# Kernel optimization log

Hardware: AMD Instinct MI355X
Metric: run time of the kernel (lower is better)

The kernel has to match this reference:

```python
import jax, jax.numpy as jnp
import numpy as np
from jax import lax

V_PATCH = (1, 2, 3, 4, 5, 6, 8, 10, 13, 16)
BETA = 0.25
RESI = 0.5          # abs(quant_resi): h*(1-r) + conv(h)*r
K_PHI = 4           # share_quant_resi
PHI_TICKS = np.linspace(1.0 / (3 * K_PHI), 1.0 - 1.0 / (3 * K_PHI), K_PHI)


def _area_mat(out_s, in_s):
    # torch F.interpolate(mode='area') == adaptive avg pool: row-stochastic matrix
    M = np.zeros((out_s, in_s), np.float32)
    for i in range(out_s):
        s = (i * in_s) // out_s
        e = -((-(i + 1) * in_s) // out_s)  # ceil((i+1)*in/out)
        M[i, s:e] = 1.0 / (e - s)
    return jnp.asarray(M)


def _bicubic_mat(out_s, in_s):
    # torch bicubic, align_corners=False, a=-0.75, border-clamped taps
    a = -0.75
    i = np.arange(out_s)
    src = (i + 0.5) * in_s / out_s - 0.5
    fl = np.floor(src)
    M = np.zeros((out_s, in_s), np.float32)
    for t in range(-1, 3):
        x = np.abs(src - (fl + t))
        w = np.where(x <= 1.0, (a + 2) * x**3 - (a + 3) * x**2 + 1.0,
                     np.where(x < 2.0, a * x**3 - 5 * a * x**2 + 8 * a * x - 4 * a, 0.0))
        idx = np.clip(fl + t, 0, in_s - 1).astype(int)
        np.add.at(M, (i, idx), w)
    return jnp.asarray(M)


def _resize(x, M):
    # separable resize on square maps: x [B,C,h,w] -> [B,C,o,o]
    x = jnp.einsum('oh,bchw->bcow', M, x)
    return jnp.einsum('pw,bcow->bcop', M, x)


def _phi(h, w, b):
    # Phi: Conv2d(C,C,3,pad=1); out = h*(1-r) + conv(h)*r
    c = lax.conv_general_dilated(h, w, (1, 1), 'SAME',
                                 dimension_numbers=('NCHW', 'OIHW', 'NCHW'))
    c = c + b[None, :, None, None]
    return h * (1.0 - RESI) + c * RESI


def setup_inputs() -> dict:
    key = jax.random.key(0)
    k1, k2, k3, k4 = jax.random.split(key, 4)
    f = jax.random.normal(k1, (128, 32, 16, 16), jnp.float32)
    emb = jax.random.normal(k2, (4096, 32), jnp.float32) * 0.1
    phi_w = jax.random.normal(k3, (4, 32, 32, 3, 3), jnp.float32) * 0.05
    phi_b = jax.random.normal(k4, (4, 32), jnp.float32) * 0.01
    return {"f_BChw": f, "emb_W": emb, "phi_W": phi_w, "phi_b": phi_b}


def reference(f_BChw, emb_W, phi_W, phi_b):
    B, C, H, W = f_BChw.shape
    SN = len(V_PATCH)
    f = f_BChw.astype(jnp.float32)
    f_ng = lax.stop_gradient(f)
    f_rest = f_ng
    f_hat = jnp.zeros_like(f_ng)
    emb_ng = lax.stop_gradient(emb_W)         # torch uses embedding.weight.data
    e_sq = jnp.sum(emb_ng**2, axis=1)          # [V]
    loss = jnp.float32(0.0)
    idx_list = []
    for si, pn in enumerate(V_PATCH):
        rest = f_rest if si == SN - 1 else _resize(f_rest, _area_mat(pn, H))
        rest_NC = rest.transpose(0, 2, 3, 1).reshape(-1, C)      # [B*pn*pn, C]
        d = jnp.sum(rest_NC**2, axis=1, keepdims=True) + e_sq - 2.0 * (rest_NC @ emb_ng.T)
        idx = jnp.argmin(d, axis=1)                              # [B*pn*pn]
        idx_list.append(idx)
        h = emb_W[idx].reshape(B, pn, pn, C).transpose(0, 3, 1, 2)  # differentiable gather
        if si != SN - 1:
            h = _resize(h, _bicubic_mat(H, pn))
        k = int(np.argmin(np.abs(PHI_TICKS - si / (SN - 1))))
        h = _phi(h, phi_W[k], phi_b[k])
        f_hat = f_hat + h
        f_rest = f_rest - h
        loss = loss + BETA * jnp.mean((lax.stop_gradient(f_hat) - f)**2) \
                    + jnp.mean((f_hat - f_ng)**2)
    loss = loss / SN
    f_hat_out = lax.stop_gradient(f_hat) - f_ng + f  # straight-through
    return (f_hat_out, loss, jnp.concatenate(idx_list))
```

## Files before the change

kernel.cpp:

```cpp
#include <hip/hip_runtime.h>
#include <hip/hip_bf16.h>
#include <math.h>


#define B_  128
#define V_  4096
#define SN_ 10
#define NPIX_ (B_*32*256)

#define WS_FREST   0
#define WS_SLOTA   1048576
#define WS_SLOTB   1114112
#define WS_ESQ     1179648
#define WS_TW      1183744
#define WS_TI      1184320
#define WS_LOSSP   1184896
#define WS_RESTH   1187456
#define WS_RESTM   1711744
#define WS_RESTL   2236032
#define WS_EMBH    2760320
#define WS_EMBM    2825856
#define WS_EMBL    2891392
#define WS_WSPL    2956928

typedef __attribute__((ext_vector_type(8))) short short8_t;
typedef __attribute__((ext_vector_type(4))) float f32x4;
typedef unsigned long long ull;
#define MFMA(a,b,c) __builtin_amdgcn_mfma_f32_16x16x32_bf16((a),(b),(c),0,0,0)

__device__ inline void gl_lds16(const void* g, void* l) {
  __builtin_amdgcn_global_load_lds((const __attribute__((address_space(1))) void*)g,
                                   (__attribute__((address_space(3))) void*)l, 16, 0, 0);
}
__device__ inline void gl_lds4(const void* g, void* l) {
  __builtin_amdgcn_global_load_lds((const __attribute__((address_space(1))) void*)g,
                                   (__attribute__((address_space(3))) void*)l, 4, 0, 0);
}

__device__ inline void split3(float a, ushort* h, ushort* m, ushort* l) {
  unsigned ua = __float_as_uint(a);
  ushort uh = (ushort)(ua >> 16);
  float fh = __uint_as_float((unsigned)uh << 16);
  float r1 = a - fh;
  ushort um = (ushort)(__float_as_uint(r1) >> 16);
  float fm = __uint_as_float((unsigned)um << 16);
  float r2 = r1 - fm;
  ushort ul = (ushort)(__float_as_uint(r2) >> 16);
  *h = uh; *m = um; *l = ul;
}

__device__ inline short8_t s8_from_laneM1(short8_t v) {
  union { short8_t s; unsigned u[4]; } a, r;
  a.s = v;
#pragma unroll
  for (int i = 0; i < 4; ++i)
    r.u[i] = __builtin_amdgcn_update_dpp(0u, a.u[i], 0x111, 0xF, 0xF, true);
  return r.s;
}
__device__ inline short8_t s8_from_laneP1(short8_t v) {
  union { short8_t s; unsigned u[4]; } a, r;
  a.s = v;
#pragma unroll
  for (int i = 0; i < 4; ++i)
    r.u[i] = __builtin_amdgcn_update_dpp(0u, a.u[i], 0x101, 0xF, 0xF, true);
  return r.s;
}


__global__ __launch_bounds__(256) void k_prep(const float* __restrict__ emb,
                                              float* __restrict__ esq,
                                              ushort* __restrict__ eh,
                                              ushort* __restrict__ em,
                                              ushort* __restrict__ el,
                                              float* __restrict__ tw,
                                              int* __restrict__ ti,
                                              ull* __restrict__ slotA) {
  int bx = blockIdx.x, t = threadIdx.x;
  if (bx < 16) {
    int v = bx * 256 + t;
    const float4* e4 = (const float4*)(emb + (size_t)v * 32);
    float s = 0.f;
#pragma unroll
    for (int half = 0; half < 4; ++half) {
      float4 x0 = e4[half * 2], x1 = e4[half * 2 + 1];
      s += x0.x * x0.x + x0.y * x0.y + x0.z * x0.z + x0.w * x0.w;
      s += x1.x * x1.x + x1.y * x1.y + x1.z * x1.z + x1.w * x1.w;
      float xs[8] = {x0.x, x0.y, x0.z, x0.w, x1.x, x1.y, x1.z, x1.w};
      ushort hs[8], ms[8], ls[8];
#pragma unroll
      for (int j = 0; j < 8; ++j) split3(xs[j], &hs[j], &ms[j], &ls[j]);
      uint4 ph, pm, pl;
      ph.x = (unsigned)hs[0] | ((unsigned)hs[1] << 16); ph.y = (unsigned)hs[2] | ((unsigned)hs[3] << 16);
      ph.z = (unsigned)hs[4] | ((unsigned)hs[5] << 16); ph.w = (unsigned)hs[6] | ((unsigned)hs[7] << 16);
      pm.x = (unsigned)ms[0] | ((unsigned)ms[1] << 16); pm.y = (unsigned)ms[2] | ((unsigned)ms[3] << 16);
      pm.z = (unsigned)ms[4] | ((unsigned)ms[5] << 16); pm.w = (unsigned)ms[6] | ((unsigned)ms[7] << 16);
      pl.x = (unsigned)ls[0] | ((unsigned)ls[1] << 16); pl.y = (unsigned)ls[2] | ((unsigned)ls[3] << 16);
      pl.z = (unsigned)ls[4] | ((unsigned)ls[5] << 16); pl.w = (unsigned)ls[6] | ((unsigned)ls[7] << 16);
      ((uint4*)(eh + (size_t)v * 32))[half] = ph;
      ((uint4*)(em + (size_t)v * 32))[half] = pm;
      ((uint4*)(el + (size_t)v * 32))[half] = pl;
    }
    esq[v] = -0.5f * s;
  } else {
    if (t < 128) slotA[t] = 0ULL;
    if (t >= 144) return;
    const int pns[9] = {1, 2, 3, 4, 5, 6, 8, 10, 13};
    int si = t / 16, Y = t % 16;
    int pn = pns[si];
    double src = (Y + 0.5) * (double)pn / 16.0 - 0.5;
    double fl = floor(src);
    const double a = -0.75;
#pragma unroll
    for (int k = 0; k < 4; ++k) {
      double x = fabs(src - (fl + (k - 1)));
      double w;
      if (x <= 1.0)      w = (a + 2.0) * x * x * x - (a + 3.0) * x * x + 1.0;
      else if (x < 2.0)  w = a * x * x * x - 5.0 * a * x * x + 8.0 * a * x - 4.0 * a;
      else               w = 0.0;
      int id = (int)fl + (k - 1);
      id = id < 0 ? 0 : (id > pn - 1 ? pn - 1 : id);
      tw[si * 64 + Y * 4 + k] = (float)w;
      ti[si * 64 + Y * 4 + k] = id;
    }
  }
}

__global__ __launch_bounds__(256) void k_prep2(const float* __restrict__ f,
                                               const float* __restrict__ phiW,
                                               ushort* __restrict__ rh,
                                               ushort* __restrict__ rm,
                                               ushort* __restrict__ rl,
                                               ushort* __restrict__ wspl) {
  int bx = blockIdx.x, t = threadIdx.x;
  if (bx < 16) {
    int i = bx * 256 + t;
    int phi = i >> 10, o = (i >> 5) & 31, ci = i & 31;
    const float* src = phiW + (((size_t)phi * 32 + o) * 32 + ci) * 9;
    ushort* dst = wspl + (size_t)phi * 27648;
#pragma unroll
    for (int q = 0; q < 9; ++q) {
      ushort uh, um, ul;
      split3(src[q], &uh, &um, &ul);
      dst[(size_t)(0 * 9 + q) * 1024 + o * 32 + ci] = uh;
      dst[(size_t)(9 + q) * 1024 + o * 32 + ci] = um;
      dst[(size_t)(18 + q) * 1024 + o * 32 + ci] = ul;
    }
  } else {
    int tid = (bx - 16) * 256 + t;
    int c = tid & 31, n = tid >> 5;
    const float* base = f + ((size_t)n * 32 + c) * 256;
    float s = 0.f;
    for (int yy = 0; yy < 16; ++yy)
      for (int xx = 0; xx < 16; ++xx) s += base[yy * 16 + xx];
    float a = s * ((1.0f / 16.0f) * (1.0f / 16.0f));
    ushort uh, um, ul;
    split3(a, &uh, &um, &ul);
    rh[(size_t)n * 32 + c] = uh;
    rm[(size_t)n * 32 + c] = um;
    rl[(size_t)n * 32 + c] = ul;
  }
}

template<int R>
__global__ __launch_bounds__(256) void k_nn(const ushort* __restrict__ rest_h,
                                            const ushort* __restrict__ rest_m,
                                            const ushort* __restrict__ rest_l,
                                            const ushort* __restrict__ emb_h,
                                            const ushort* __restrict__ emb_m,
                                            const ushort* __restrict__ emb_l,
                                            const float* __restrict__ esq_g,
                                            ull* __restrict__ slot,
                                            int rows, int S, int cps) {
  __shared__ ushort lb[2][3][2048];
  __shared__ float les[2][64];
  const int t = threadIdx.x;
  const int w = t >> 6;
  const int col = t & 15;
  const int g = (t >> 4) & 3;
  const int sp = blockIdx.y;
  const int rowbase = blockIdx.x * (64 * R);

  auto stage = [&](int bf, int ch) {
    int cb = sp * cps + ch * 64;
    int code = cb + (t >> 2);
    int u = (t & 3) ^ ((code ^ (code >> 2)) & 3);
    size_t off = (size_t)code * 32 + (size_t)u * 8;
    gl_lds16(emb_h + off, &lb[bf][0][w * 512]);
    gl_lds16(emb_m + off, &lb[bf][1][w * 512]);
    gl_lds16(emb_l + off, &lb[bf][2][w * 512]);
    if ((t & 63) < 16) gl_lds4(esq_g + cb + w * 16 + (t & 15), &les[bf][w * 16]);
  };

  stage(0, 0);

  short8_t ah[R], am[R], al[R];
#pragma unroll
  for (int rt = 0; rt < R; ++rt) {
    int n = rowbase + (w * R + rt) * 16 + col;
    if (n >= rows) n = rows - 1;
    size_t o = (size_t)n * 32 + g * 8;
    ah[rt] = *(const short8_t*)(rest_h + o);
    am[rt] = *(const short8_t*)(rest_m + o);
    al[rt] = *(const short8_t*)(rest_l + o);
  }

  float best[R][4];
  int bidx[R][4];
#pragma unroll
  for (int rt = 0; rt < R; ++rt)
#pragma unroll
    for (int r = 0; r < 4; ++r) { best[rt][r] = -3.4e38f; bidx[rt][r] = 0x7fffffff; }

  const int NC = cps >> 6;
  int buf = 0;
  for (int ch = 0; ch < NC; ++ch) {
    if (ch + 1 < NC) {
      stage(buf ^ 1, ch + 1);
      asm volatile("s_waitcnt vmcnt(4)" ::: "memory");
    } else {
      asm volatile("s_waitcnt vmcnt(0)" ::: "memory");
    }
    __builtin_amdgcn_s_barrier();

    int cb0 = sp * cps + ch * 64;
#pragma unroll
    for (int s4 = 0; s4 < 4; ++s4) {
      int cl = s4 * 16 + col;
      int slotbase = (cl * 4 + (g ^ ((cl ^ (cl >> 2)) & 3))) * 8;
      short8_t bh  = *(const short8_t*)&lb[buf][0][slotbase];
      short8_t bm  = *(const short8_t*)&lb[buf][1][slotbase];
      short8_t bl2 = *(const short8_t*)&lb[buf][2][slotbase];
      float es = les[buf][cl];
      f32x4 c0 = {es, es, es, es};
      f32x4 acc[R];
#pragma unroll
      for (int rt = 0; rt < R; ++rt) acc[rt] = MFMA(ah[rt], bh, c0);
#pragma unroll
      for (int rt = 0; rt < R; ++rt) acc[rt] = MFMA(ah[rt], bm, acc[rt]);
#pragma unroll
      for (int rt = 0; rt < R; ++rt) acc[rt] = MFMA(am[rt], bh, acc[rt]);
#pragma unroll
      for (int rt = 0; rt < R; ++rt) acc[rt] = MFMA(ah[rt], bl2, acc[rt]);
#pragma unroll
      for (int rt = 0; rt < R; ++rt) acc[rt] = MFMA(am[rt], bm, acc[rt]);
#pragma unroll
      for (int rt = 0; rt < R; ++rt) acc[rt] = MFMA(al[rt], bh, acc[rt]);
      int code = cb0 + cl;
#pragma unroll
      for (int rt = 0; rt < R; ++rt)
#pragma unroll
        for (int r = 0; r < 4; ++r)
          if (acc[rt][r] > best[rt][r]) { best[rt][r] = acc[rt][r]; bidx[rt][r] = code; }
    }
    __syncthreads();
    buf ^= 1;
  }

#pragma unroll
  for (int rt = 0; rt < R; ++rt)
#pragma unroll
    for (int r = 0; r < 4; ++r) {
      float bd = best[rt][r];
      int bi = bidx[rt][r];
#pragma unroll
      for (int mm2 = 1; mm2 < 16; mm2 <<= 1) {
        float od = __shfl_xor(bd, mm2, 16);
        int oi = __shfl_xor(bi, mm2, 16);
        if (od > bd || (od == bd && oi < bi)) { bd = od; bi = oi; }
      }
      if ((t & 15) == 0) {
        int rown = rowbase + (w * R + rt) * 16 + g * 4 + r;
        if (rown < rows) {
          unsigned mu = __float_as_uint(bd);
          mu ^= (mu & 0x80000000u) ? 0xFFFFFFFFu : 0x80000000u;
          ull key = ((ull)mu << 32) | (unsigned)(~bi);
          atomicMax(&slot[rown], key);
        }
      }
    }
}

template<bool LAST>
__global__ __launch_bounds__(1024) void k_scale(const ull* __restrict__ slot_in,
                                                ull* __restrict__ slot_next,
                                                const float* __restrict__ emb,
                                                const float* __restrict__ tw,
                                                const int* __restrict__ ti,
                                                const ushort* __restrict__ wspl,
                                                const float* __restrict__ bias,
                                                const float* __restrict__ f,
                                                const float* __restrict__ fr_in,
                                                float* __restrict__ fr_out,
                                                float* __restrict__ fhat_out,
                                                float* __restrict__ out_idx_f,
                                                float* __restrict__ lossp,
                                                ushort* __restrict__ rh,
                                                ushort* __restrict__ rm,
                                                ushort* __restrict__ rl,
                                                int pn, int si, int pn_next,
                                                int rows_next) {
  __shared__ ushort h_bf[3][256][40];
  __shared__ float hsm[32 * 177];
  __shared__ float xt[32][208];
  __shared__ float h_my[16][260];
  __shared__ ushort w_lds[27][16][36];
  __shared__ int ci_s[256];
  __shared__ float redw[16];
  float* poolb = hsm;

  const int b = blockIdx.x;
  const int cog = blockIdx.y * 16;
  const int t = threadIdx.x;
  const int pn2 = pn * pn;
  const int w = t >> 6, l = t & 63;
  const int X = l & 15, kq = l >> 4;
  const int pix = w * 16 + X;

  float fr_old[4], f_old[4];
#pragma unroll
  for (int r = 0; r < 4; ++r) {
    size_t ga = ((size_t)b * 32 + cog + kq * 4 + r) * 256 + pix;
    fr_old[r] = fr_in[ga];
    f_old[r] = LAST ? f[ga] : 0.f;
  }
  for (int i = t; i < 1728; i += 1024) {
    int seg = i & 3;
    int o = (i >> 2) & 15;
    int lq = i >> 6;
    const ushort* src = wspl + ((size_t)lq * 32 + cog + o) * 32 + seg * 8;
    *(short8_t*)&w_lds[lq][o][seg * 8] = *(const short8_t*)src;
  }
  for (int rem = t; rem < pn2; rem += 1024) {
    ull sv = slot_in[b * pn2 + rem];
    int code = (int)(~(unsigned)sv);
    ci_s[rem] = code;
    out_idx_f[b * pn2 + rem] = (float)code;
  }
  __syncthreads();

  if (LAST) {
    const float4* emb4 = (const float4*)emb;
    for (int i = t; i < 2048; i += 1024) {
      int p2 = i >> 3, cq = i & 7;
      float4 e = emb4[(size_t)ci_s[p2] * 8 + cq];
      float vs[4] = {e.x, e.y, e.z, e.w};
#pragma unroll
      for (int j = 0; j < 4; ++j) {
        int c = cq * 4 + j;
        ushort uh, um, ul; split3(vs[j], &uh, &um, &ul);
        h_bf[0][p2][c] = uh; h_bf[1][p2][c] = um; h_bf[2][p2][c] = ul;
        int cl = c - cog;
        if ((unsigned)cl < 16u) h_my[cl][p2] = vs[j];
      }
    }
    __syncthreads();
  } else {
    const float4* emb4 = (const float4*)emb;
    for (int i = t; i < pn2 * 8; i += 1024) {
      int rem = i >> 3, cq = i & 7;
      float4 e = emb4[(size_t)ci_s[rem] * 8 + cq];
      hsm[(cq * 4 + 0) * 177 + rem] = e.x;
      hsm[(cq * 4 + 1) * 177 + rem] = e.y;
      hsm[(cq * 4 + 2) * 177 + rem] = e.z;
      hsm[(cq * 4 + 3) * 177 + rem] = e.w;
    }
    __syncthreads();

#pragma unroll
    for (int cc = 0; cc < 2; ++cc) {
      int c = 2 * w + cc;
      for (int i = l; i < pn * 16; i += 64) {
        int Xi = i & 15, y = i >> 4;
        float a = 0.f;
#pragma unroll
        for (int u = 0; u < 4; ++u)
          a += tw[si * 64 + Xi * 4 + u] * hsm[c * 177 + y * pn + ti[si * 64 + Xi * 4 + u]];
        xt[c][y * 16 + Xi] = a;
      }
      asm volatile("s_waitcnt lgkmcnt(0)" ::: "memory");
      for (int p2 = l; p2 < 256; p2 += 64) {
        int Xi = p2 & 15, Y = p2 >> 4;
        float a = 0.f;
#pragma unroll
        for (int u = 0; u < 4; ++u)
          a += tw[si * 64 + Y * 4 + u] * xt[c][ti[si * 64 + Y * 4 + u] * 16 + Xi];
        ushort uh, um, ul; split3(a, &uh, &um, &ul);
        h_bf[0][p2][c] = uh; h_bf[1][p2][c] = um; h_bf[2][p2][c] = ul;
        int cl = c - cog;
        if ((unsigned)cl < 16u) h_my[cl][p2] = a;
      }
    }
    __syncthreads();
  }

  f32x4 accA, accB;
#pragma unroll
  for (int r = 0; r < 4; ++r) {
    accA[r] = bias[cog + kq * 4 + r];
    accB[r] = 0.f;
  }

  for (int dy = 0; dy < 3; ++dy) {
    int Yp = w + dy - 1;
    bool ok = (Yp >= 0 && Yp < 16);
    short8_t bc[3];
    if (ok) {
#pragma unroll
      for (int lv = 0; lv < 3; ++lv)
        bc[lv] = *(const short8_t*)&h_bf[lv][Yp * 16 + X][kq * 8];
    }
#pragma unroll
    for (int dx = 0; dx < 3; ++dx) {
      int q = dy * 3 + dx;
      short8_t aH = *(const short8_t*)&w_lds[0 * 9 + q][l & 15][kq * 8];
      short8_t aM = *(const short8_t*)&w_lds[9 + q][l & 15][kq * 8];
      short8_t aL = *(const short8_t*)&w_lds[18 + q][l & 15][kq * 8];
      if (!ok) continue;
      short8_t bH = bc[0], bM = bc[1], bL = bc[2];
      if (dx == 0) { bH = s8_from_laneM1(bH); bM = s8_from_laneM1(bM); bL = s8_from_laneM1(bL); }
      else if (dx == 2) { bH = s8_from_laneP1(bH); bM = s8_from_laneP1(bM); bL = s8_from_laneP1(bL); }
      accA = MFMA(aH, bH, accA);
      accB = MFMA(aH, bM, accB);
      accA = MFMA(aM, bH, accA);
      accB = MFMA(aH, bL, accB);
      accA = MFMA(aM, bM, accA);
      accB = MFMA(aL, bH, accB);
    }
  }

  float lsum = 0.f;
#pragma unroll
  for (int r = 0; r < 4; ++r) {
    int ol = kq * 4 + r;
    float convv = accA[r] + accB[r];
    float outv = 0.5f * h_my[ol][pix] + 0.5f * convv;
    float nf = fr_old[r] - outv;
    size_t ga = ((size_t)b * 32 + cog + ol) * 256 + pix;
    if (LAST) {
      fhat_out[ga] = f_old[r] - nf;
    } else {
      fr_out[ga] = nf;
      poolb[ol * 256 + pix] = nf;
    }
    lsum += nf * nf;
  }

  if (!LAST) {
    __syncthreads();
    int pn2n = pn_next * pn_next;
    for (int i = t; i < 16 * pn2n; i += 1024) {
      int o = i & 15, rem = i >> 4;
      int y = rem / pn_next, x = rem - y * pn_next;
      int sy = (y * 16) / pn_next, ey = ((y + 1) * 16 + pn_next - 1) / pn_next;
      int sx = (x * 16) / pn_next, ex = ((x + 1) * 16 + pn_next - 1) / pn_next;
      float s = 0.f;
      for (int yy = sy; yy < ey; ++yy)
        for (int xx = sx; xx < ex; ++xx) s += poolb[o * 256 + yy * 16 + xx];
      float a = s * ((1.0f / (float)(ey - sy)) * (1.0f / (float)(ex - sx)));
      ushort uh, um, ul;
      split3(a, &uh, &um, &ul);
      size_t n = (size_t)b * pn2n + rem;
      rh[n * 32 + cog + o] = uh;
      rm[n * 32 + cog + o] = um;
      rl[n * 32 + cog + o] = ul;
    }
    int blk = b * 2 + blockIdx.y;
    int stride = (rows_next + 255) >> 8;
    int base = blk * stride;
    for (int i = t; i < stride; i += 1024) {
      int s = base + i;
      if (s < rows_next) slot_next[s] = 0ULL;
    }
  }

#pragma unroll
  for (int off = 32; off > 0; off >>= 1) lsum += __shfl_down(lsum, off);
  if (l == 0) redw[w] = lsum;
  __syncthreads();
  if (t == 0) {
    float s2 = 0.f;
#pragma unroll
    for (int i = 0; i < 16; ++i) s2 += redw[i];
    lossp[si * 256 + blockIdx.y * 128 + b] = s2;
  }
}

__global__ __launch_bounds__(256) void k_lossfin(const float* __restrict__ part,
                                                 float* __restrict__ out) {
  int t = threadIdx.x;
  float s = 0.f;
  for (int i = t; i < SN_ * 256; i += 256) s += part[i];
  __shared__ float red[256];
  red[t] = s;
  __syncthreads();
  for (int o = 128; o > 0; o >>= 1) {
    if (t < o) red[t] += red[t + o];
    __syncthreads();
  }
  if (t == 0) out[NPIX_] = red[0] * (1.25f / (10.0f * (float)NPIX_));
}


static void compute_phi_k(int* ks) {
  const int K = 4;
  double start = 1.0 / (3.0 * K);
  double stop = 1.0 - 1.0 / (3.0 * K);
  double step = (stop - start) / (K - 1);
  double ticks[4];
  for (int i = 0; i < K; ++i) ticks[i] = (double)i * step + start;
  ticks[K - 1] = stop;
  for (int si = 0; si < SN_; ++si) {
    double x = (double)si / (SN_ - 1);
    int best = 0;
    double bd = fabs(ticks[0] - x);
    for (int i = 1; i < K; ++i) {
      double d = fabs(ticks[i] - x);
      if (d < bd) { bd = d; best = i; }
    }
    ks[si] = best;
  }
}

extern "C" void kernel_launch(void* const* d_in, const int* in_sizes, int n_in,
                              void* d_out, int out_size, void* d_ws, size_t ws_size,
                              hipStream_t stream) {
  (void)in_sizes; (void)n_in; (void)out_size; (void)ws_size;
  const float* f    = (const float*)d_in[0];
  const float* emb  = (const float*)d_in[1];
  const float* phiW = (const float*)d_in[2];
  const float* phiB = (const float*)d_in[3];
  float* out = (float*)d_out;
  float* ws = (float*)d_ws;

  float* f_rest = ws + WS_FREST;
  ull*   slotA  = (ull*)(ws + WS_SLOTA);
  ull*   slotB  = (ull*)(ws + WS_SLOTB);
  float* esq    = ws + WS_ESQ;
  float* tw     = ws + WS_TW;
  int*   ti     = (int*)(ws + WS_TI);
  float* lossp  = ws + WS_LOSSP;
  ushort* rest_h = (ushort*)(ws + WS_RESTH);
  ushort* rest_m = (ushort*)(ws + WS_RESTM);
  ushort* rest_l = (ushort*)(ws + WS_RESTL);
  ushort* emb_h  = (ushort*)(ws + WS_EMBH);
  ushort* emb_m  = (ushort*)(ws + WS_EMBM);
  ushort* emb_l  = (ushort*)(ws + WS_EMBL);
  ushort* wspl   = (ushort*)(ws + WS_WSPL);

  static const int pns[SN_] = {1, 2, 3, 4, 5, 6, 8, 10, 13, 16};
  static const int Rs[SN_]  = {1, 1, 1, 2, 2, 2, 4, 4, 4, 4};
  static const int Ss[SN_]  = {64, 64, 32, 32, 16, 16, 16, 16, 8, 4};
  int ks[SN_];
  compute_phi_k(ks);

  k_prep<<<17, 256, 0, stream>>>(emb, esq, emb_h, emb_m, emb_l, tw, ti, slotA);
  k_prep2<<<32, 256, 0, stream>>>(f, phiW, rest_h, rest_m, rest_l, wspl);

  int idx_off = 0;
  for (int si = 0; si < SN_; ++si) {
    int pn = pns[si];
    int pn2 = pn * pn;
    int rows = B_ * pn2;
    int R = Rs[si], S = Ss[si];
    int cps = V_ / S;
    int rowblocks = (rows + 64 * R - 1) / (64 * R);
    ull* slot_cur  = (si & 1) ? slotB : slotA;
    ull* slot_nxt  = (si & 1) ? slotA : slotB;

    dim3 grid(rowblocks, S);
    if (R == 1)
      k_nn<1><<<grid, 256, 0, stream>>>(rest_h, rest_m, rest_l, emb_h, emb_m, emb_l,
                                        esq, slot_cur, rows, S, cps);
    else if (R == 2)
      k_nn<2><<<grid, 256, 0, stream>>>(rest_h, rest_m, rest_l, emb_h, emb_m, emb_l,
                                        esq, slot_cur, rows, S, cps);
    else
      k_nn<4><<<grid, 256, 0, stream>>>(rest_h, rest_m, rest_l, emb_h, emb_m, emb_l,
                                        esq, slot_cur, rows, S, cps);

    bool last = (si == SN_ - 1);
    int pn_next = last ? 0 : pns[si + 1];
    int rows_next = last ? 0 : B_ * pn_next * pn_next;
    const ushort* wsp = wspl + (size_t)ks[si] * 27648;
    const float* bi = phiB + (size_t)ks[si] * 32;
    if (last)
      k_scale<true><<<dim3(B_, 2), 1024, 0, stream>>>(
          slot_cur, slot_nxt, emb, tw, ti, wsp, bi, f,
          f_rest, f_rest, out,
          out + NPIX_ + 1 + idx_off, lossp,
          rest_h, rest_m, rest_l, pn, si, pn_next, rows_next);
    else
      k_scale<false><<<dim3(B_, 2), 1024, 0, stream>>>(
          slot_cur, slot_nxt, emb, tw, ti, wsp, bi, f,
          (si == 0) ? f : f_rest, f_rest, nullptr,
          out + NPIX_ + 1 + idx_off, lossp,
          rest_h, rest_m, rest_l, pn, si, pn_next, rows_next);
    idx_off += rows;
  }

  k_lossfin<<<1, 256, 0, stream>>>(lossp, out);
}
```

Before: 363.5 us.

## Split k_scale by image half, use fp32 rest with atomic area-pool accumulation

```diff
diff --git a/kernel.cpp b/kernel.cpp
--- a/kernel.cpp
+++ b/kernel.cpp
@@ -9,19 +9,18 @@
 #define NPIX_ (B_*32*256)
 
 #define WS_FREST   0
-#define WS_SLOTA   1048576
-#define WS_SLOTB   1114112
-#define WS_ESQ     1179648
-#define WS_TW      1183744
-#define WS_TI      1184320
-#define WS_LOSSP   1184896
-#define WS_RESTH   1187456
-#define WS_RESTM   1711744
-#define WS_RESTL   2236032
-#define WS_EMBH    2760320
-#define WS_EMBM    2825856
-#define WS_EMBL    2891392
-#define WS_WSPL    2956928
+#define WS_RF0     1048576
+#define WS_RF1     2097152
+#define WS_SLOTA   3145728
+#define WS_SLOTB   3211264
+#define WS_ESQ     3276800
+#define WS_TW      3280896
+#define WS_TI      3281472
+#define WS_LOSSP   3282048
+#define WS_EMBH    3287168
+#define WS_EMBM    3352704
+#define WS_EMBL    3418240
+#define WS_WSPL    3483776
 
 typedef __attribute__((ext_vector_type(8))) short short8_t;
 typedef __attribute__((ext_vector_type(4))) float f32x4;
@@ -74,7 +73,8 @@
                                               ushort* __restrict__ el,
                                               float* __restrict__ tw,
                                               int* __restrict__ ti,
-                                              ull* __restrict__ slotA) {
+                                              ull* __restrict__ slotA,
+                                              float* __restrict__ rf1) {
   int bx = blockIdx.x, t = threadIdx.x;
   if (bx < 16) {
     int v = bx * 256 + t;
@@ -103,6 +103,7 @@
     esq[v] = -0.5f * s;
   } else {
     if (t < 128) slotA[t] = 0ULL;
+    for (int i = t; i < 16384; i += 256) rf1[i] = 0.f;
     if (t >= 144) return;
     const int pns[9] = {1, 2, 3, 4, 5, 6, 8, 10, 13};
     int si = t / 16, Y = t % 16;
@@ -127,9 +128,7 @@
 
 __global__ __launch_bounds__(256) void k_prep2(const float* __restrict__ f,
                                                const float* __restrict__ phiW,
-                                               ushort* __restrict__ rh,
-                                               ushort* __restrict__ rm,
-                                               ushort* __restrict__ rl,
+                                               float* __restrict__ rf0,
                                                ushort* __restrict__ wspl) {
   int bx = blockIdx.x, t = threadIdx.x;
   if (bx < 16) {
@@ -152,19 +151,12 @@
     float s = 0.f;
     for (int yy = 0; yy < 16; ++yy)
       for (int xx = 0; xx < 16; ++xx) s += base[yy * 16 + xx];
-    float a = s * ((1.0f / 16.0f) * (1.0f / 16.0f));
-    ushort uh, um, ul;
-    split3(a, &uh, &um, &ul);
-    rh[(size_t)n * 32 + c] = uh;
-    rm[(size_t)n * 32 + c] = um;
-    rl[(size_t)n * 32 + c] = ul;
+    rf0[(size_t)n * 32 + c] = s * ((1.0f / 16.0f) * (1.0f / 16.0f));
   }
 }
 
 template<int R>
-__global__ __launch_bounds__(256) void k_nn(const ushort* __restrict__ rest_h,
-                                            const ushort* __restrict__ rest_m,
-                                            const ushort* __restrict__ rest_l,
+__global__ __launch_bounds__(256) void k_nn(const float* __restrict__ rest_f,
                                             const ushort* __restrict__ emb_h,
                                             const ushort* __restrict__ emb_m,
                                             const ushort* __restrict__ emb_l,
@@ -198,10 +190,14 @@
   for (int rt = 0; rt < R; ++rt) {
     int n = rowbase + (w * R + rt) * 16 + col;
     if (n >= rows) n = rows - 1;
-    size_t o = (size_t)n * 32 + g * 8;
-    ah[rt] = *(const short8_t*)(rest_h + o);
-    am[rt] = *(const short8_t*)(rest_m + o);
-    al[rt] = *(const short8_t*)(rest_l + o);
+    const float* rf = rest_f + (size_t)n * 32 + g * 8;
+    f32x4 v0 = *(const f32x4*)rf;
+    f32x4 v1 = *(const f32x4*)(rf + 4);
+    float vs[8] = {v0[0], v0[1], v0[2], v0[3], v1[0], v1[1], v1[2], v1[3]};
+    union { ushort u[8]; short8_t s; } H, M, L;
+#pragma unroll
+    for (int j = 0; j < 8; ++j) split3(vs[j], &H.u[j], &M.u[j], &L.u[j]);
+    ah[rt] = H.s; am[rt] = M.s; al[rt] = L.s;
   }
 
   float best[R][4];
@@ -281,41 +277,48 @@
 }
 
 template<bool LAST>
-__global__ __launch_bounds__(1024) void k_scale(const ull* __restrict__ slot_in,
-                                                ull* __restrict__ slot_next,
-                                                const float* __restrict__ emb,
-                                                const float* __restrict__ tw,
-                                                const int* __restrict__ ti,
-                                                const ushort* __restrict__ wspl,
-                                                const float* __restrict__ bias,
-                                                const float* __restrict__ f,
-                                                const float* __restrict__ fr_in,
-                                                float* __restrict__ fr_out,
-                                                float* __restrict__ fhat_out,
-                                                float* __restrict__ out_idx_f,
-                                                float* __restrict__ lossp,
-                                                ushort* __restrict__ rh,
-                                                ushort* __restrict__ rm,
-                                                ushort* __restrict__ rl,
-                                                int pn, int si, int pn_next,
-                                                int rows_next) {
-  __shared__ ushort h_bf[3][256][40];
-  __shared__ float hsm[32 * 177];
-  __shared__ float xt[32][208];
-  __shared__ float h_my[16][260];
+__global__ __launch_bounds__(512, 4) void k_scale(const ull* __restrict__ slot_in,
+                                                  ull* __restrict__ slot_next,
+                                                  float* __restrict__ rest_next,
+                                                  float* __restrict__ rest_zero,
+                                                  const float* __restrict__ emb,
+                                                  const float* __restrict__ tw,
+                                                  const int* __restrict__ ti,
+                                                  const ushort* __restrict__ wspl_k,
+                                                  const float* __restrict__ bias,
+                                                  const float* __restrict__ f,
+                                                  const float* __restrict__ fr_in,
+                                                  float* __restrict__ fr_out,
+                                                  float* __restrict__ fhat_out,
+                                                  float* __restrict__ out_idx_f,
+                                                  float* __restrict__ lossp,
+                                                  int pn, int si, int pn_next,
+                                                  int rows_next, int rows_z2) {
+  __shared__ ushort h_bf[3][144][32];
+  __shared__ float xt8[8][208];
+  __shared__ float hsm8[8][176];
+  __shared__ float h_my[16][128];
   __shared__ ushort w_lds[27][16][36];
   __shared__ int ci_s[256];
-  __shared__ float redw[16];
-  float* poolb = hsm;
+  __shared__ float redw[8];
 
   const int b = blockIdx.x;
   const int cog = blockIdx.y * 16;
+  const int z = blockIdx.z;
   const int t = threadIdx.x;
   const int pn2 = pn * pn;
   const int w = t >> 6, l = t & 63;
   const int X = l & 15, kq = l >> 4;
-  const int pix = w * 16 + X;
-
+  const int grow = z * 8 + w;
+  const int pix = grow * 16 + X;
+  const int rowbase = z ? 7 : 0;
+
+  for (int rem = t; rem < pn2; rem += 512) {
+    ull sv = slot_in[b * pn2 + rem];
+    int code = (int)(~(unsigned)sv);
+    ci_s[rem] = code;
+    if (blockIdx.y == 0 && z == 0) out_idx_f[b * pn2 + rem] = (float)code;
+  }
   float fr_old[4], f_old[4];
 #pragma unroll
   for (int r = 0; r < 4; ++r) {
@@ -323,74 +326,77 @@
     fr_old[r] = fr_in[ga];
     f_old[r] = LAST ? f[ga] : 0.f;
   }
-  for (int i = t; i < 1728; i += 1024) {
+  for (int i = t; i < 1728; i += 512) {
     int seg = i & 3;
     int o = (i >> 2) & 15;
     int lq = i >> 6;
-    const ushort* src = wspl + ((size_t)lq * 32 + cog + o) * 32 + seg * 8;
+    const ushort* src = wspl_k + ((size_t)lq * 32 + cog + o) * 32 + seg * 8;
     *(short8_t*)&w_lds[lq][o][seg * 8] = *(const short8_t*)src;
-  }
-  for (int rem = t; rem < pn2; rem += 1024) {
-    ull sv = slot_in[b * pn2 + rem];
-    int code = (int)(~(unsigned)sv);
-    ci_s[rem] = code;
-    out_idx_f[b * pn2 + rem] = (float)code;
   }
   __syncthreads();
 
   if (LAST) {
     const float4* emb4 = (const float4*)emb;
-    for (int i = t; i < 2048; i += 1024) {
-      int p2 = i >> 3, cq = i & 7;
-      float4 e = emb4[(size_t)ci_s[p2] * 8 + cq];
+    for (int i = t; i < 1152; i += 512) {
+      int lp = i % 144, cq = i / 144;
+      int gp = rowbase * 16 + lp;
+      float4 e = emb4[(size_t)ci_s[gp] * 8 + cq];
       float vs[4] = {e.x, e.y, e.z, e.w};
 #pragma unroll
       for (int j = 0; j < 4; ++j) {
         int c = cq * 4 + j;
         ushort uh, um, ul; split3(vs[j], &uh, &um, &ul);
-        h_bf[0][p2][c] = uh; h_bf[1][p2][c] = um; h_bf[2][p2][c] = ul;
+        int sc = (c & 7) + (((c >> 3) ^ (lp & 3)) << 3);
+        h_bf[0][lp][sc] = uh; h_bf[1][lp][sc] = um; h_bf[2][lp][sc] = ul;
+        int grr = rowbase + (lp >> 4);
         int cl = c - cog;
-        if ((unsigned)cl < 16u) h_my[cl][p2] = vs[j];
+        if ((unsigned)cl < 16u && (grr >> 3) == z)
+          h_my[cl][(grr - z * 8) * 16 + (lp & 15)] = vs[j];
       }
     }
     __syncthreads();
   } else {
     const float4* emb4 = (const float4*)emb;
-    for (int i = t; i < pn2 * 8; i += 1024) {
-      int rem = i >> 3, cq = i & 7;
-      float4 e = emb4[(size_t)ci_s[rem] * 8 + cq];
-      hsm[(cq * 4 + 0) * 177 + rem] = e.x;
-      hsm[(cq * 4 + 1) * 177 + rem] = e.y;
-      hsm[(cq * 4 + 2) * 177 + rem] = e.z;
-      hsm[(cq * 4 + 3) * 177 + rem] = e.w;
-    }
-    __syncthreads();
-
-#pragma unroll
-    for (int cc = 0; cc < 2; ++cc) {
-      int c = 2 * w + cc;
-      for (int i = l; i < pn * 16; i += 64) {
-        int Xi = i & 15, y = i >> 4;
+#pragma unroll 1
+    for (int P = 0; P < 4; ++P) {
+      for (int i = t; i < pn2 * 2; i += 512) {
+        int rem = i >> 1, hf = i & 1;
+        float4 e = emb4[(size_t)ci_s[rem] * 8 + P * 2 + hf];
+        hsm8[hf * 4 + 0][rem] = e.x;
+        hsm8[hf * 4 + 1][rem] = e.y;
+        hsm8[hf * 4 + 2][rem] = e.z;
+        hsm8[hf * 4 + 3][rem] = e.w;
+      }
+      __syncthreads();
+      int e1n = 8 * pn * 16;
+      for (int i = t; i < e1n; i += 512) {
+        int Xi = i & 15, r2 = i >> 4;
+        int y = r2 % pn, c8 = r2 / pn;
         float a = 0.f;
 #pragma unroll
         for (int u = 0; u < 4; ++u)
-          a += tw[si * 64 + Xi * 4 + u] * hsm[c * 177 + y * pn + ti[si * 64 + Xi * 4 + u]];
-        xt[c][y * 16 + Xi] = a;
-      }
-      asm volatile("s_waitcnt lgkmcnt(0)" ::: "memory");
-      for (int p2 = l; p2 < 256; p2 += 64) {
-        int Xi = p2 & 15, Y = p2 >> 4;
+          a += tw[si * 64 + Xi * 4 + u] * hsm8[c8][y * pn + ti[si * 64 + Xi * 4 + u]];
+        xt8[c8][y * 16 + Xi] = a;
+      }
+      __syncthreads();
+      for (int i = t; i < 1152; i += 512) {
+        int lp = i % 144, c8 = i / 144;
+        int Xi = lp & 15, lr = lp >> 4;
+        int gY = rowbase + lr;
         float a = 0.f;
 #pragma unroll
         for (int u = 0; u < 4; ++u)
-          a += tw[si * 64 + Y * 4 + u] * xt[c][ti[si * 64 + Y * 4 + u] * 16 + Xi];
+          a += tw[si * 64 + gY * 4 + u] * xt8[c8][ti[si * 64 + gY * 4 + u] * 16 + Xi];
+        int c = P * 8 + c8;
         ushort uh, um, ul; split3(a, &uh, &um, &ul);
-        h_bf[0][p2][c] = uh; h_bf[1][p2][c] = um; h_bf[2][p2][c] = ul;
+        int sc = (c & 7) + (((c >> 3) ^ (lp & 3)) << 3);
+        h_bf[0][lp][sc] = uh; h_bf[1][lp][sc] = um; h_bf[2][lp][sc] = ul;
         int cl = c - cog;
-        if ((unsigned)cl < 16u) h_my[cl][p2] = a;
-      }
-    }
-    __syncthreads();
+        if ((unsigned)cl < 16u && (gY >> 3) == z)
+          h_my[cl][(gY - z * 8) * 16 + Xi] = a;
+      }
+      __syncthreads();
+    }
   }
 
   f32x4 accA, accB;
@@ -401,13 +407,15 @@
   }
 
   for (int dy = 0; dy < 3; ++dy) {
-    int Yp = w + dy - 1;
-    bool ok = (Yp >= 0 && Yp < 16);
+    int gYp = grow + dy - 1;
+    bool ok = (gYp >= 0 && gYp < 16);
     short8_t bc[3];
     if (ok) {
+      int lp = (gYp - rowbase) * 16 + X;
+      int sc = ((kq ^ (lp & 3)) << 3);
 #pragma unroll
       for (int lv = 0; lv < 3; ++lv)
-        bc[lv] = *(const short8_t*)&h_bf[lv][Yp * 16 + X][kq * 8];
+        bc[lv] = *(const short8_t*)&h_bf[lv][lp][sc];
     }
 #pragma unroll
     for (int dx = 0; dx < 3; ++dx) {
@@ -428,48 +436,64 @@
     }
   }
 
+  float nf_r[4];
   float lsum = 0.f;
 #pragma unroll
   for (int r = 0; r < 4; ++r) {
     int ol = kq * 4 + r;
     float convv = accA[r] + accB[r];
-    float outv = 0.5f * h_my[ol][pix] + 0.5f * convv;
+    float outv = 0.5f * h_my[ol][w * 16 + X] + 0.5f * convv;
     float nf = fr_old[r] - outv;
     size_t ga = ((size_t)b * 32 + cog + ol) * 256 + pix;
     if (LAST) {
       fhat_out[ga] = f_old[r] - nf;
     } else {
       fr_out[ga] = nf;
-      poolb[ol * 256 + pix] = nf;
-    }
+    }
+    nf_r[r] = nf;
     lsum += nf * nf;
   }
 
   if (!LAST) {
     __syncthreads();
+    float* poolb = &h_my[0][0];
+#pragma unroll
+    for (int r = 0; r < 4; ++r)
+      poolb[(kq * 4 + r) * 128 + w * 16 + X] = nf_r[r];
+    __syncthreads();
     int pn2n = pn_next * pn_next;
-    for (int i = t; i < 16 * pn2n; i += 1024) {
+    int z8 = z * 8;
+    for (int i = t; i < 16 * pn2n; i += 512) {
       int o = i & 15, rem = i >> 4;
       int y = rem / pn_next, x = rem - y * pn_next;
       int sy = (y * 16) / pn_next, ey = ((y + 1) * 16 + pn_next - 1) / pn_next;
       int sx = (x * 16) / pn_next, ex = ((x + 1) * 16 + pn_next - 1) / pn_next;
+      int lsy = sy > z8 ? sy : z8;
+      int ley = ey < z8 + 8 ? ey : z8 + 8;
+      if (lsy >= ley) continue;
       float s = 0.f;
-      for (int yy = sy; yy < ey; ++yy)
-        for (int xx = sx; xx < ex; ++xx) s += poolb[o * 256 + yy * 16 + xx];
-      float a = s * ((1.0f / (float)(ey - sy)) * (1.0f / (float)(ex - sx)));
-      ushort uh, um, ul;
-      split3(a, &uh, &um, &ul);
-      size_t n = (size_t)b * pn2n + rem;
-      rh[n * 32 + cog + o] = uh;
-      rm[n * 32 + cog + o] = um;
-      rl[n * 32 + cog + o] = ul;
-    }
-    int blk = b * 2 + blockIdx.y;
-    int stride = (rows_next + 255) >> 8;
-    int base = blk * stride;
-    for (int i = t; i < stride; i += 1024) {
-      int s = base + i;
-      if (s < rows_next) slot_next[s] = 0ULL;
+      for (int yy = lsy; yy < ley; ++yy)
+        for (int xx = sx; xx < ex; ++xx) s += poolb[o * 128 + (yy - z8) * 16 + xx];
+      float val = s * ((1.0f / (float)(ey - sy)) * (1.0f / (float)(ex - sx)));
+      atomicAdd(&rest_next[(size_t)(b * pn2n + rem) * 32 + cog + o], val);
+    }
+    int blk = (z * 2 + blockIdx.y) * 128 + b;
+    if (rows_z2 > 0) {
+      int tot = rows_z2 * 32;
+      int stride = (tot + 511) >> 9;
+      int base = blk * stride;
+      for (int i = t; i < stride; i += 512) {
+        int s = base + i;
+        if (s < tot) rest_zero[s] = 0.f;
+      }
+    }
+    {
+      int stride = (rows_next + 511) >> 9;
+      int base = blk * stride;
+      for (int i = t; i < stride; i += 512) {
+        int s = base + i;
+        if (s < rows_next) slot_next[s] = 0ULL;
+      }
     }
   }
 
@@ -480,8 +504,8 @@
   if (t == 0) {
     float s2 = 0.f;
 #pragma unroll
-    for (int i = 0; i < 16; ++i) s2 += redw[i];
-    lossp[si * 256 + blockIdx.y * 128 + b] = s2;
+    for (int i = 0; i < 8; ++i) s2 += redw[i];
+    lossp[si * 512 + (z * 2 + blockIdx.y) * 128 + b] = s2;
   }
 }
 
@@ -489,7 +513,7 @@
                                                  float* __restrict__ out) {
   int t = threadIdx.x;
   float s = 0.f;
-  for (int i = t; i < SN_ * 256; i += 256) s += part[i];
+  for (int i = t; i < SN_ * 512; i += 256) s += part[i];
   __shared__ float red[256];
   red[t] = s;
   __syncthreads();
@@ -533,15 +557,14 @@
   float* ws = (float*)d_ws;
 
   float* f_rest = ws + WS_FREST;
+  float* rf0    = ws + WS_RF0;
+  float* rf1    = ws + WS_RF1;
   ull*   slotA  = (ull*)(ws + WS_SLOTA);
   ull*   slotB  = (ull*)(ws + WS_SLOTB);
   float* esq    = ws + WS_ESQ;
   float* tw     = ws + WS_TW;
   int*   ti     = (int*)(ws + WS_TI);
   float* lossp  = ws + WS_LOSSP;
-  ushort* rest_h = (ushort*)(ws + WS_RESTH);
-  ushort* rest_m = (ushort*)(ws + WS_RESTM);
-  ushort* rest_l = (ushort*)(ws + WS_RESTL);
   ushort* emb_h  = (ushort*)(ws + WS_EMBH);
   ushort* emb_m  = (ushort*)(ws + WS_EMBM);
   ushort* emb_l  = (ushort*)(ws + WS_EMBL);
@@ -553,8 +576,8 @@
   int ks[SN_];
   compute_phi_k(ks);
 
-  k_prep<<<17, 256, 0, stream>>>(emb, esq, emb_h, emb_m, emb_l, tw, ti, slotA);
-  k_prep2<<<32, 256, 0, stream>>>(f, phiW, rest_h, rest_m, rest_l, wspl);
+  k_prep<<<17, 256, 0, stream>>>(emb, esq, emb_h, emb_m, emb_l, tw, ti, slotA, rf1);
+  k_prep2<<<32, 256, 0, stream>>>(f, phiW, rf0, wspl);
 
   int idx_off = 0;
   for (int si = 0; si < SN_; ++si) {
@@ -564,37 +587,40 @@
     int R = Rs[si], S = Ss[si];
     int cps = V_ / S;
     int rowblocks = (rows + 64 * R - 1) / (64 * R);
-    ull* slot_cur  = (si & 1) ? slotB : slotA;
-    ull* slot_nxt  = (si & 1) ? slotA : slotB;
+    ull* slot_cur = (si & 1) ? slotB : slotA;
+    ull* slot_nxt = (si & 1) ? slotA : slotB;
+    float* rest_cur = (si & 1) ? rf1 : rf0;
+    float* rest_nxt = (si & 1) ? rf0 : rf1;
 
     dim3 grid(rowblocks, S);
     if (R == 1)
-      k_nn<1><<<grid, 256, 0, stream>>>(rest_h, rest_m, rest_l, emb_h, emb_m, emb_l,
+      k_nn<1><<<grid, 256, 0, stream>>>(rest_cur, emb_h, emb_m, emb_l,
                                         esq, slot_cur, rows, S, cps);
     else if (R == 2)
-      k_nn<2><<<grid, 256, 0, stream>>>(rest_h, rest_m, rest_l, emb_h, emb_m, emb_l,
+      k_nn<2><<<grid, 256, 0, stream>>>(rest_cur, emb_h, emb_m, emb_l,
                                         esq, slot_cur, rows, S, cps);
     else
-      k_nn<4><<<grid, 256, 0, stream>>>(rest_h, rest_m, rest_l, emb_h, emb_m, emb_l,
+      k_nn<4><<<grid, 256, 0, stream>>>(rest_cur, emb_h, emb_m, emb_l,
                                         esq, slot_cur, rows, S, cps);
 
     bool last = (si == SN_ - 1);
     int pn_next = last ? 0 : pns[si + 1];
     int rows_next = last ? 0 : B_ * pn_next * pn_next;
+    int rows_z2 = (si + 2 <= SN_ - 1) ? B_ * pns[si + 2] * pns[si + 2] : 0;
     const ushort* wsp = wspl + (size_t)ks[si] * 27648;
     const float* bi = phiB + (size_t)ks[si] * 32;
     if (last)
-      k_scale<true><<<dim3(B_, 2), 1024, 0, stream>>>(
-          slot_cur, slot_nxt, emb, tw, ti, wsp, bi, f,
+      k_scale<true><<<dim3(B_, 2, 2), 512, 0, stream>>>(
+          slot_cur, slot_nxt, rest_nxt, rest_cur, emb, tw, ti, wsp, bi, f,
           f_rest, f_rest, out,
           out + NPIX_ + 1 + idx_off, lossp,
-          rest_h, rest_m, rest_l, pn, si, pn_next, rows_next);
+          pn, si, pn_next, rows_next, rows_z2);
     else
-      k_scale<false><<<dim3(B_, 2), 1024, 0, stream>>>(
-          slot_cur, slot_nxt, emb, tw, ti, wsp, bi, f,
+      k_scale<false><<<dim3(B_, 2, 2), 512, 0, stream>>>(
+          slot_cur, slot_nxt, rest_nxt, rest_cur, emb, tw, ti, wsp, bi, f,
           (si == 0) ? f : f_rest, f_rest, nullptr,
           out + NPIX_ + 1 + idx_off, lossp,
-          rest_h, rest_m, rest_l, pn, si, pn_next, rows_next);
+          pn, si, pn_next, rows_next, rows_z2);
     idx_off += rows;
   }
 
```

Result: slower. 375.7 us (+3.4%).
